# Kernel tuning notes

Hardware: AMD Instinct MI355X
Metric: run time of the kernel (lower is better)

## Reference

```python
import jax, jax.numpy as jnp
import numpy as np

B, S, E = 4, 1024, 1024
H = 16
HD = E // H  # 64
NEXP = 8
FF = 4 * E
EPS = 1e-5


def _ln(x, g, b):
    m = jnp.mean(x, axis=-1, keepdims=True)
    v = jnp.var(x, axis=-1, keepdims=True)
    return (x - m) * jax.lax.rsqrt(v + EPS) * g + b


def setup_inputs() -> dict:
    key = jax.random.key(0)
    ks = jax.random.split(key, 16)
    sd = 0.02
    inp = {
        "x": jax.random.normal(ks[0], (B, S, E), jnp.float32),
        # per-head Q/K/V linears, stacked over heads: [H, E, HD]
        "wq": jax.random.normal(ks[1], (H, E, HD), jnp.float32) * sd,
        "bq": jnp.zeros((H, HD), jnp.float32),
        "wk": jax.random.normal(ks[2], (H, E, HD), jnp.float32) * sd,
        "bk": jnp.zeros((H, HD), jnp.float32),
        "wv": jax.random.normal(ks[3], (H, E, HD), jnp.float32) * sd,
        "bv": jnp.zeros((H, HD), jnp.float32),
        "wp": jax.random.normal(ks[4], (E, E), jnp.float32) * sd,
        "bp": jnp.zeros((E,), jnp.float32),
        "ln1_g": jnp.ones((E,), jnp.float32),
        "ln1_b": jnp.zeros((E,), jnp.float32),
        "ln2_g": jnp.ones((E,), jnp.float32),
        "ln2_b": jnp.zeros((E,), jnp.float32),
        "wr": jax.random.normal(ks[5], (E, NEXP), jnp.float32) * sd,
        "br": jnp.zeros((NEXP,), jnp.float32),
        # experts stacked: [NEXP, E, FF], [NEXP, FF, E]
        "w1": jax.random.normal(ks[6], (NEXP, E, FF), jnp.float32) * sd,
        "b1": jnp.zeros((NEXP, FF), jnp.float32),
        "w2": jax.random.normal(ks[7], (NEXP, FF, E), jnp.float32) * sd,
        "b2": jnp.zeros((NEXP, E), jnp.float32),
    }
    return inp


def _block(x, wq, bq, wk, bk, wv, bv, wp, bp, ln1_g, ln1_b, ln2_g, ln2_b,
           wr, br, w1, b1, w2, b2):
    # --- multi-head causal attention (per-head Q/K/V, concat, project) ---
    q = jnp.einsum('bse,hed->bhsd', x, wq) + bq[None, :, None, :]
    k = jnp.einsum('bse,hed->bhsd', x, wk) + bk[None, :, None, :]
    v = jnp.einsum('bse,hed->bhsd', x, wv) + bv[None, :, None, :]
    scores = jnp.einsum('bhsd,bhtd->bhst', q, k) / jnp.sqrt(jnp.float32(HD))
    causal = jnp.tril(jnp.ones((S, S), bool))
    scores = jnp.where(causal[None, None], scores, -jnp.inf)
    attn = jax.nn.softmax(scores, axis=-1)
    heads = jnp.einsum('bhst,bhtd->bhsd', attn, v)
    # concat heads (dim order matches torch.cat over head list)
    cat = heads.transpose(0, 2, 1, 3).reshape(B, S, E)
    attn_out = cat @ wp + bp
    # --- residual + LN1 ---
    h = _ln(attn_out + x, ln1_g, ln1_b)
    # --- MoE: router probs weight ALL experts densely (indices unused) ---
    probs = jax.nn.softmax(h @ wr + br, axis=-1)  # [B,S,NEXP]
    mid = jax.nn.relu(jnp.einsum('bse,nef->bnsf', h, w1) + b1[None, :, None, :])
    eo = jnp.einsum('bnsf,nfe->bnse', mid, w2) + b2[None, :, None, :]
    moe_out = jnp.einsum('bnse,bsn->bse', eo, probs)
    # --- residual uses ORIGINAL inputs (as in source) + LN2 ---
    return _ln(moe_out + x, ln2_g, ln2_b)


def reference(x, wq, bq, wk, bk, wv, bv, wp, bp, ln1_g, ln1_b, ln2_g, ln2_b,
              wr, br, w1, b1, w2, b2):
    return _block(x, wq, bq, wk, bk, wv, bv, wp, bp, ln1_g, ln1_b,
                  ln2_g, ln2_b, wr, br, w1, b1, w2, b2)
```

## Files before the change

### kernel.cpp

```cpp
#include <hip/hip_runtime.h>
#include <hip/hip_bf16.h>

typedef unsigned short u16;
typedef unsigned int u32;
typedef __attribute__((ext_vector_type(8))) short bf16x8;
typedef __attribute__((ext_vector_type(4))) float f32x4;

#define DEV static __device__ __forceinline__

DEV u16 f2b(float f) {
  union { float f; u32 u; } v; v.f = f;
  return (u16)((v.u + 0x7fffu + ((v.u >> 16) & 1u)) >> 16);
}

DEV void gload16(const void* g, void* l) {
  __builtin_amdgcn_global_load_lds(
      (const __attribute__((address_space(1))) u32*)g,
      (__attribute__((address_space(3))) u32*)l, 16, 0, 0);
}

__global__ __launch_bounds__(256) void cvt_bf16(const float* __restrict__ s,
                                                u16* __restrict__ d) {
  const long i = ((long)blockIdx.x * 256 + threadIdx.x) * 4;
  const float4 v = *(const float4*)&s[i];
  ushort4 o;
  o.x = f2b(v.x); o.y = f2b(v.y); o.z = f2b(v.z); o.w = f2b(v.w);
  *(ushort4*)&d[i] = o;
}

__global__ __launch_bounds__(256) void tpose_bf16(const float* __restrict__ src,
                                                  u16* __restrict__ dst, int R,
                                                  int C, long sStride,
                                                  long dStride, long ldd) {
  __shared__ float tl[32][33];
  const float* s = src + (long)blockIdx.z * sStride;
  u16* d = dst + (long)blockIdx.z * dStride;
  const int c0 = blockIdx.x * 32, r0 = blockIdx.y * 32;
  const int tx = threadIdx.x, ty = threadIdx.y;
#pragma unroll
  for (int k = 0; k < 4; k++)
    tl[ty + k * 8][tx] = s[(long)(r0 + ty + k * 8) * C + c0 + tx];
  __syncthreads();
#pragma unroll
  for (int k = 0; k < 4; k++)
    d[(long)(c0 + ty + k * 8) * ldd + r0 + tx] = f2b(tl[tx][ty + k * 8]);
}

enum { EQKV, EPROJ, EFF1, EFF2, EFF2I };

template <int EPI>
__global__ __launch_bounds__(256, 2) void gemm_bt(
    const u16* __restrict__ A, const u16* __restrict__ Bt, int K, long lda,
    long ldb, const float* __restrict__ c0, const float* __restrict__ c1,
    const float* __restrict__ c2, const float* __restrict__ aux,
    float* __restrict__ fout, u16* __restrict__ o0, u16* __restrict__ o1,
    u16* __restrict__ o2, int ebase, long ldc) {
  __shared__ u16 As[8192], Bs[8192];
  long zc = 0;
  if constexpr (EPI == EFF2 || EPI == EFF2I) {
    const long z = blockIdx.z;
    A += z * (long)K;
    Bt += z * (long)K;
    fout += z * 4194304;
  }
  if constexpr (EPI == EFF1) {
    Bt += (long)blockIdx.z * 4194304;
    zc = (long)blockIdx.z * 4096;
  }
  const int tid = threadIdx.x;
  const int m0 = blockIdx.y * 128, n0 = blockIdx.x * 128;
  const int w = tid >> 6, l = tid & 63;
  const int wm = (w >> 1) * 64, wn = (w & 1) * 64;
  const int lr = l & 15, lh = l >> 4;
  f32x4 acc[4][4] = {};
  const u16* Ag = A + (long)(m0 + (tid >> 3)) * lda + (tid & 7) * 8;
  const u16* Bg = Bt + (long)(n0 + (tid >> 3)) * ldb + (tid & 7) * 8;
  for (int kt = 0; kt < K; kt += 64) {
    __syncthreads();
    gload16(Ag, As + tid * 8);
    gload16(Ag + 32 * lda, As + tid * 8 + 2048);
    gload16(Ag + 64 * lda, As + tid * 8 + 4096);
    gload16(Ag + 96 * lda, As + tid * 8 + 6144);
    gload16(Bg, Bs + tid * 8);
    gload16(Bg + 32 * ldb, Bs + tid * 8 + 2048);
    gload16(Bg + 64 * ldb, Bs + tid * 8 + 4096);
    gload16(Bg + 96 * ldb, Bs + tid * 8 + 6144);
    Ag += 64; Bg += 64;
    __syncthreads();
#pragma unroll
    for (int kk = 0; kk < 2; kk++) {
      bf16x8 af[4], bfr[4];
#pragma unroll
      for (int i = 0; i < 4; i++)
        af[i] = *(const bf16x8*)&As[(wm + i * 16 + lr) * 64 + kk * 32 + lh * 8];
#pragma unroll
      for (int j = 0; j < 4; j++)
        bfr[j] = *(const bf16x8*)&Bs[(wn + j * 16 + lr) * 64 + kk * 32 + lh * 8];
#pragma unroll
      for (int i = 0; i < 4; i++)
#pragma unroll
        for (int j = 0; j < 4; j++)
          acc[i][j] = __builtin_amdgcn_mfma_f32_16x16x32_bf16(
              af[i], bfr[j], acc[i][j], 0, 0, 0);
    }
  }
#pragma unroll
  for (int j = 0; j < 4; j++) {
    const int col = n0 + wn + j * 16 + lr;
#pragma unroll
    for (int i = 0; i < 4; i++)
#pragma unroll
      for (int r = 0; r < 4; r++) {
        const int row = m0 + wm + i * 16 + lh * 4 + r;
        float v = acc[i][j][r];
        if constexpr (EPI == EQKV) {
          const int which = col >> 10, hd = col & 1023;
          const float vb =
              v + ((which == 0) ? c0 : (which == 1) ? c1 : c2)[hd];
          const int b = row >> 10, s = row & 1023;
          const int h = hd >> 6, d = hd & 63;
          const long bh = b * 16 + h;
          if (which == 0)
            o0[(bh * 1024 + s) * 64 + d] = f2b(vb * 0.125f);
          else if (which == 1)
            o1[(bh * 1024 + s) * 64 + d] = f2b(vb);
          else
            o2[bh * 65536 + (long)d * 1024 + s] = f2b(vb);
        } else if constexpr (EPI == EPROJ) {
          const long idx = (long)row * 1024 + col;
          fout[idx] = v + c0[col] + aux[idx];
        } else if constexpr (EPI == EFF1) {
          const int e = ebase + blockIdx.z;
          const float t = v + c0[(long)e * 4096 + col];
          const float rl = t > 0.f ? t : 0.f;
          const float pw = aux[(long)row * 8 + e];
          o0[(long)row * ldc + zc + col] = f2b(rl * pw);
        } else {
          const long idx = (long)row * 1024 + col;
          if constexpr (EPI == EFF2I)
            fout[idx] = v;
          else
            fout[idx] = fout[idx] + v;
        }
      }
  }
}

__global__ __launch_bounds__(256) void attn_fwd(const u16* __restrict__ Qb,
                                                const u16* __restrict__ Kb,
                                                const u16* __restrict__ Vt,
                                                u16* __restrict__ Cat) {
  const int tid = threadIdx.x;
  const int w = tid >> 6, l = tid & 63;
  const int lr = l & 15, lh = l >> 4;
  const int bh = blockIdx.y;
  const int q0 = blockIdx.x * 64 + w * 16;
  const u16* Qp = Qb + (long)bh * 65536;
  const u16* Kp = Kb + (long)bh * 65536;
  const u16* Vp = Vt + (long)bh * 65536;
  const bf16x8 qf0 = *(const bf16x8*)&Qp[(q0 + lr) * 64 + lh * 8];
  const bf16x8 qf1 = *(const bf16x8*)&Qp[(q0 + lr) * 64 + 32 + lh * 8];
  const int q = q0 + lr;
  f32x4 o[4] = {};
  float m = -1e30f, ssum = 0.f;
  const int hi = lh >> 1;
  const int s0 = ((lh & 1) * 2) * 16 + lr;
  const int s1 = ((lh & 1) * 2 + 1) * 16 + lr;
  const int nkt = q0 / 32 + 1;
  for (int kt = 0; kt < nkt; kt++) {
    const int t0 = kt * 32;
    f32x4 sc[2];
#pragma unroll
    for (int ts = 0; ts < 2; ts++) {
      const bf16x8 kf0 = *(const bf16x8*)&Kp[(t0 + ts * 16 + lr) * 64 + lh * 8];
      const bf16x8 kf1 =
          *(const bf16x8*)&Kp[(t0 + ts * 16 + lr) * 64 + 32 + lh * 8];
      f32x4 c = {};
      c = __builtin_amdgcn_mfma_f32_16x16x32_bf16(kf0, qf0, c, 0, 0, 0);
      c = __builtin_amdgcn_mfma_f32_16x16x32_bf16(kf1, qf1, c, 0, 0, 0);
      sc[ts] = c;
    }
#pragma unroll
    for (int ts = 0; ts < 2; ts++)
#pragma unroll
      for (int r = 0; r < 4; r++)
        if (t0 + ts * 16 + lh * 4 + r > q) sc[ts][r] = -1e30f;
    float mt = fmaxf(fmaxf(fmaxf(sc[0][0], sc[0][1]), fmaxf(sc[0][2], sc[0][3])),
                     fmaxf(fmaxf(sc[1][0], sc[1][1]), fmaxf(sc[1][2], sc[1][3])));
    mt = fmaxf(mt, __shfl_xor(mt, 16));
    mt = fmaxf(mt, __shfl_xor(mt, 32));
    const float mnew = fmaxf(m, mt);
    const float scl = __expf(m - mnew);
    m = mnew;
    float p0[4], p1[4], ps = 0.f;
#pragma unroll
    for (int r = 0; r < 4; r++) {
      p0[r] = __expf(sc[0][r] - mnew);
      p1[r] = __expf(sc[1][r] - mnew);
      ps += p0[r] + p1[r];
    }
    ssum = ssum * scl + ps;
    u16 pb[8];
#pragma unroll
    for (int r = 0; r < 4; r++) {
      const float a0 = __shfl(p0[r], s0), b0 = __shfl(p1[r], s0);
      const float a1 = __shfl(p0[r], s1), b1 = __shfl(p1[r], s1);
      pb[r] = f2b(hi ? b0 : a0);
      pb[r + 4] = f2b(hi ? b1 : a1);
    }
#pragma unroll
    for (int dt = 0; dt < 4; dt++)
#pragma unroll
      for (int r = 0; r < 4; r++) o[dt][r] *= scl;
    const bf16x8 pf = *(const bf16x8*)pb;
    __builtin_amdgcn_s_setprio(1);
#pragma unroll
    for (int dt = 0; dt < 4; dt++) {
      const bf16x8 vf =
          *(const bf16x8*)&Vp[(dt * 16 + lr) * 1024 + t0 + lh * 8];
      o[dt] = __builtin_amdgcn_mfma_f32_16x16x32_bf16(vf, pf, o[dt], 0, 0, 0);
    }
    __builtin_amdgcn_s_setprio(0);
  }
  ssum += __shfl_xor(ssum, 16);
  ssum += __shfl_xor(ssum, 32);
  const float inv = 1.f / ssum;
  const int b = bh >> 4, h = bh & 15;
#pragma unroll
  for (int dt = 0; dt < 4; dt++) {
    ushort4 st;
    st.x = f2b(o[dt][0] * inv);
    st.y = f2b(o[dt][1] * inv);
    st.z = f2b(o[dt][2] * inv);
    st.w = f2b(o[dt][3] * inv);
    *(ushort4*)&Cat[((long)(b * 1024 + q)) * 1024 + h * 64 + dt * 16 + lh * 4] =
        st;
  }
}

DEV float wred(float v) {
#pragma unroll
  for (int d = 1; d < 64; d <<= 1) v += __shfl_xor(v, d);
  return v;
}

__global__ __launch_bounds__(256) void ln1_router(
    const float* __restrict__ in, const float* __restrict__ g,
    const float* __restrict__ bb, const float* __restrict__ wr,
    const float* __restrict__ br, u16* __restrict__ h,
    float* __restrict__ probs) {
  __shared__ float rs[4], rs2[4], rp[4][8];
  const int row = blockIdx.x, t = threadIdx.x;
  const int w = t >> 6, l = t & 63;
  const float4 v = *(const float4*)&in[(long)row * 1024 + t * 4];
  float s = v.x + v.y + v.z + v.w;
  float s2 = v.x * v.x + v.y * v.y + v.z * v.z + v.w * v.w;
  s = wred(s);
  s2 = wred(s2);
  if (l == 0) { rs[w] = s; rs2[w] = s2; }
  __syncthreads();
  const float S = rs[0] + rs[1] + rs[2] + rs[3];
  const float S2 = rs2[0] + rs2[1] + rs2[2] + rs2[3];
  const float mean = S * (1.f / 1024.f);
  const float var = S2 * (1.f / 1024.f) - mean * mean;
  const float rr = rsqrtf(var + 1e-5f);
  const float4 gv = *(const float4*)&g[t * 4];
  const float4 bv = *(const float4*)&bb[t * 4];
  float hv[4];
  hv[0] = (v.x - mean) * rr * gv.x + bv.x;
  hv[1] = (v.y - mean) * rr * gv.y + bv.y;
  hv[2] = (v.z - mean) * rr * gv.z + bv.z;
  hv[3] = (v.w - mean) * rr * gv.w + bv.w;
  ushort4 hb;
  hb.x = f2b(hv[0]); hb.y = f2b(hv[1]); hb.z = f2b(hv[2]); hb.w = f2b(hv[3]);
  *(ushort4*)&h[(long)row * 1024 + t * 4] = hb;
  float pr[8] = {};
  const float* wrp = wr + t * 4 * 8;
#pragma unroll
  for (int e = 0; e < 4; e++)
#pragma unroll
    for (int j = 0; j < 8; j++) pr[j] += hv[e] * wrp[e * 8 + j];
#pragma unroll
  for (int j = 0; j < 8; j++) pr[j] = wred(pr[j]);
  if (l == 0)
#pragma unroll
    for (int j = 0; j < 8; j++) rp[w][j] = pr[j];
  __syncthreads();
  if (t == 0) {
    float lg[8], mx = -1e30f;
#pragma unroll
    for (int j = 0; j < 8; j++) {
      lg[j] = rp[0][j] + rp[1][j] + rp[2][j] + rp[3][j] + br[j];
      mx = fmaxf(mx, lg[j]);
    }
    float sm = 0.f;
#pragma unroll
    for (int j = 0; j < 8; j++) {
      lg[j] = __expf(lg[j] - mx);
      sm += lg[j];
    }
    const float inv = 1.f / sm;
#pragma unroll
    for (int j = 0; j < 8; j++) probs[row * 8 + j] = lg[j] * inv;
  }
}

__global__ __launch_bounds__(256) void ln2_kernel(
    const float* __restrict__ moe, const float* __restrict__ xres,
    const float* __restrict__ probs, const float* __restrict__ b2,
    const float* __restrict__ g, const float* __restrict__ bb,
    float* __restrict__ out, int np) {
  __shared__ float rs[4], rs2[4];
  const int row = blockIdx.x, t = threadIdx.x;
  const int w = t >> 6, l = t & 63;
  const long base = (long)row * 1024 + t * 4;
  float4 v = *(const float4*)&xres[base];
  for (int z = 0; z < np; z++) {
    const float4 a = *(const float4*)&moe[(long)z * 4194304 + base];
    v.x += a.x; v.y += a.y; v.z += a.z; v.w += a.w;
  }
#pragma unroll
  for (int n = 0; n < 8; n++) {
    const float pw = probs[(long)row * 8 + n];
    const float4 bv4 = *(const float4*)&b2[n * 1024 + t * 4];
    v.x += pw * bv4.x; v.y += pw * bv4.y;
    v.z += pw * bv4.z; v.w += pw * bv4.w;
  }
  float s = v.x + v.y + v.z + v.w;
  float s2 = v.x * v.x + v.y * v.y + v.z * v.z + v.w * v.w;
  s = wred(s);
  s2 = wred(s2);
  if (l == 0) { rs[w] = s; rs2[w] = s2; }
  __syncthreads();
  const float S = rs[0] + rs[1] + rs[2] + rs[3];
  const float S2 = rs2[0] + rs2[1] + rs2[2] + rs2[3];
  const float mean = S * (1.f / 1024.f);
  const float var = S2 * (1.f / 1024.f) - mean * mean;
  const float rr = rsqrtf(var + 1e-5f);
  const float4 gv = *(const float4*)&g[t * 4];
  const float4 bv = *(const float4*)&bb[t * 4];
  float4 oo;
  oo.x = (v.x - mean) * rr * gv.x + bv.x;
  oo.y = (v.y - mean) * rr * gv.y + bv.y;
  oo.z = (v.z - mean) * rr * gv.z + bv.z;
  oo.w = (v.w - mean) * rr * gv.w + bv.w;
  *(float4*)&out[base] = oo;
}

extern "C" void kernel_launch(void* const* d_in, const int* in_sizes, int n_in,
                              void* d_out, int out_size, void* d_ws,
                              size_t ws_size, hipStream_t stream) {
  const float* x = (const float*)d_in[0];
  const float* wq = (const float*)d_in[1];
  const float* bq = (const float*)d_in[2];
  const float* wk = (const float*)d_in[3];
  const float* bk = (const float*)d_in[4];
  const float* wv = (const float*)d_in[5];
  const float* bv = (const float*)d_in[6];
  const float* wp = (const float*)d_in[7];
  const float* bp = (const float*)d_in[8];
  const float* g1 = (const float*)d_in[9];
  const float* be1 = (const float*)d_in[10];
  const float* g2 = (const float*)d_in[11];
  const float* be2 = (const float*)d_in[12];
  const float* wr = (const float*)d_in[13];
  const float* br = (const float*)d_in[14];
  const float* w1 = (const float*)d_in[15];
  const float* b1 = (const float*)d_in[16];
  const float* w2 = (const float*)d_in[17];
  const float* b2 = (const float*)d_in[18];
  float* out = (float*)d_out;

  char* p = (char*)d_ws;
  auto alloc = [&](size_t bytes) {
    char* r = p;
    p += (bytes + 255) & ~(size_t)255;
    return r;
  };
  u16* w1t = (u16*)alloc(67108864);
  u16* w2t2 = (u16*)alloc(67108864);
  u16* hb = (u16*)alloc(8388608);
  float* probs = (float*)alloc(131072);
  float* moe = (float*)alloc(33554432);
  float* resid1 = (float*)alloc(16777216);
  u16* xb = (u16*)alloc(8388608);
  u16* wqkvt = (u16*)alloc(6291456);
  u16* wpt = (u16*)alloc(2097152);
  u16* qb = (u16*)alloc(8388608);
  u16* kb = (u16*)alloc(8388608);
  u16* vt = (u16*)alloc(8388608);
  u16* cat = (u16*)alloc(8388608);
  const size_t need_fast = (size_t)((char*)qb - (char*)d_ws) + (size_t)268435456;
  const bool fast = ws_size >= need_fast;

  const dim3 tb(32, 8);
  cvt_bf16<<<4096, 256, 0, stream>>>(x, xb);
  tpose_bf16<<<dim3(2, 32, 16), tb, 0, stream>>>(wq, wqkvt, 1024, 64, 65536, 65536, 1024);
  tpose_bf16<<<dim3(2, 32, 16), tb, 0, stream>>>(wk, wqkvt + 1048576, 1024, 64, 65536, 65536, 1024);
  tpose_bf16<<<dim3(2, 32, 16), tb, 0, stream>>>(wv, wqkvt + 2097152, 1024, 64, 65536, 65536, 1024);
  tpose_bf16<<<dim3(32, 32, 1), tb, 0, stream>>>(wp, wpt, 1024, 1024, 0, 0, 1024);
  tpose_bf16<<<dim3(128, 32, 8), tb, 0, stream>>>(w1, w1t, 1024, 4096, 4194304, 4194304, 1024);
  tpose_bf16<<<dim3(32, 128, 8), tb, 0, stream>>>(w2, w2t2, 4096, 1024, 4194304, 4096, 32768);

  gemm_bt<EQKV><<<dim3(24, 32), 256, 0, stream>>>(
      xb, wqkvt, 1024, 1024, 1024, bq, bk, bv, nullptr, nullptr, qb, kb, vt,
      0, 0);
  attn_fwd<<<dim3(16, 64), 256, 0, stream>>>(qb, kb, vt, cat);
  gemm_bt<EPROJ><<<dim3(8, 32), 256, 0, stream>>>(
      cat, wpt, 1024, 1024, 1024, bp, nullptr, nullptr, x, resid1, nullptr,
      nullptr, nullptr, 0, 0);
  ln1_router<<<4096, 256, 0, stream>>>(resid1, g1, be1, wr, br, hb, probs);

  if (fast) {
    u16* mid = qb;
    gemm_bt<EFF1><<<dim3(32, 32, 8), 256, 0, stream>>>(
        hb, w1t, 1024, 1024, 1024, b1, nullptr, nullptr, probs, nullptr, mid,
        nullptr, nullptr, 0, 32768);
    gemm_bt<EFF2I><<<dim3(8, 32, 4), 256, 0, stream>>>(
        mid, w2t2, 8192, 32768, 32768, nullptr, nullptr, nullptr, nullptr,
        moe, nullptr, nullptr, nullptr, 0, 0);
    ln2_kernel<<<4096, 256, 0, stream>>>(moe, x, probs, b2, g2, be2, out, 4);
  } else {
    u16* mid = qb;
    for (int n = 0; n < 8; n++) {
      gemm_bt<EFF1><<<dim3(32, 32, 1), 256, 0, stream>>>(
          hb, w1t + (long)n * 4194304, 1024, 1024, 1024, b1, nullptr, nullptr,
          probs, nullptr, mid, nullptr, nullptr, n, 4096);
      if (n == 0)
        gemm_bt<EFF2I><<<dim3(8, 32, 2), 256, 0, stream>>>(
            mid, w2t2 + (long)n * 4096, 2048, 4096, 32768, nullptr, nullptr,
            nullptr, nullptr, moe, nullptr, nullptr, nullptr, 0, 0);
      else
        gemm_bt<EFF2><<<dim3(8, 32, 2), 256, 0, stream>>>(
            mid, w2t2 + (long)n * 4096, 2048, 4096, 32768, nullptr, nullptr,
            nullptr, nullptr, moe, nullptr, nullptr, nullptr, 0, 0);
    }
    ln2_kernel<<<4096, 256, 0, stream>>>(moe, x, probs, b2, g2, be2, out, 2);
  }
}
```

Baseline: 1.525 ms.

## Triple-buffer GEMM LDS with async prefetch and vectorize transpose stores

The GEMM main loop now keeps three 32-wide K slices in LDS and prefetches two tiles ahead with global_load_lds. It uses vmcnt waits and a single barrier per iteration instead of two, so global loads can overlap the MFMA work. It also raises launch bounds to 3 blocks per CU, sets wave priority around the MFMA block, and changes the transpose kernel to write 4 bf16 per thread as a vector. The cost is more LDS per block, a tighter register budget, and a fragile hand-written wait/barrier schedule that can race if the vmcnt counts are wrong.

```diff
diff --git a/kernel.cpp b/kernel.cpp
--- a/kernel.cpp
+++ b/kernel.cpp
@@ -37,25 +37,30 @@
   u16* d = dst + (long)blockIdx.z * dStride;
   const int c0 = blockIdx.x * 32, r0 = blockIdx.y * 32;
   const int tx = threadIdx.x, ty = threadIdx.y;
+  const int tid = ty * 32 + tx;
 #pragma unroll
   for (int k = 0; k < 4; k++)
     tl[ty + k * 8][tx] = s[(long)(r0 + ty + k * 8) * C + c0 + tx];
   __syncthreads();
-#pragma unroll
-  for (int k = 0; k < 4; k++)
-    d[(long)(c0 + ty + k * 8) * ldd + r0 + tx] = f2b(tl[tx][ty + k * 8]);
+  const int oc = tid >> 3, orb = (tid & 7) * 4;
+  ushort4 o;
+  o.x = f2b(tl[orb + 0][oc]);
+  o.y = f2b(tl[orb + 1][oc]);
+  o.z = f2b(tl[orb + 2][oc]);
+  o.w = f2b(tl[orb + 3][oc]);
+  *(ushort4*)&d[(long)(c0 + oc) * ldd + r0 + orb] = o;
 }
 
 enum { EQKV, EPROJ, EFF1, EFF2, EFF2I };
 
 template <int EPI>
-__global__ __launch_bounds__(256, 2) void gemm_bt(
+__global__ __launch_bounds__(256, 3) void gemm_bt(
     const u16* __restrict__ A, const u16* __restrict__ Bt, int K, long lda,
     long ldb, const float* __restrict__ c0, const float* __restrict__ c1,
     const float* __restrict__ c2, const float* __restrict__ aux,
     float* __restrict__ fout, u16* __restrict__ o0, u16* __restrict__ o1,
     u16* __restrict__ o2, int ebase, long ldc) {
-  __shared__ u16 As[8192], Bs[8192];
+  __shared__ u16 As[12288], Bs[12288];
   long zc = 0;
   if constexpr (EPI == EFF2 || EPI == EFF2I) {
     const long z = blockIdx.z;
@@ -73,37 +78,49 @@
   const int wm = (w >> 1) * 64, wn = (w & 1) * 64;
   const int lr = l & 15, lh = l >> 4;
   f32x4 acc[4][4] = {};
-  const u16* Ag = A + (long)(m0 + (tid >> 3)) * lda + (tid & 7) * 8;
-  const u16* Bg = Bt + (long)(n0 + (tid >> 3)) * ldb + (tid & 7) * 8;
-  for (int kt = 0; kt < K; kt += 64) {
-    __syncthreads();
-    gload16(Ag, As + tid * 8);
-    gload16(Ag + 32 * lda, As + tid * 8 + 2048);
-    gload16(Ag + 64 * lda, As + tid * 8 + 4096);
-    gload16(Ag + 96 * lda, As + tid * 8 + 6144);
-    gload16(Bg, Bs + tid * 8);
-    gload16(Bg + 32 * ldb, Bs + tid * 8 + 2048);
-    gload16(Bg + 64 * ldb, Bs + tid * 8 + 4096);
-    gload16(Bg + 96 * ldb, Bs + tid * 8 + 6144);
-    Ag += 64; Bg += 64;
-    __syncthreads();
-#pragma unroll
-    for (int kk = 0; kk < 2; kk++) {
-      bf16x8 af[4], bfr[4];
-#pragma unroll
-      for (int i = 0; i < 4; i++)
-        af[i] = *(const bf16x8*)&As[(wm + i * 16 + lr) * 64 + kk * 32 + lh * 8];
+  const u16* AgB = A + (long)(m0 + (tid >> 2)) * lda + (tid & 3) * 8;
+  const u16* BgB = Bt + (long)(n0 + (tid >> 2)) * ldb + (tid & 3) * 8;
+  const long rsA = 64 * lda, rsB = 64 * ldb;
+  u16* asd = As + tid * 8;
+  u16* bsd = Bs + tid * 8;
+  const int nt = K >> 5;
+  gload16(AgB, asd);             gload16(AgB + rsA, asd + 2048);
+  gload16(BgB, bsd);             gload16(BgB + rsB, bsd + 2048);
+  gload16(AgB + 32, asd + 4096); gload16(AgB + rsA + 32, asd + 6144);
+  gload16(BgB + 32, bsd + 4096); gload16(BgB + rsB + 32, bsd + 6144);
+  asm volatile("s_waitcnt vmcnt(4)" ::: "memory");
+  __builtin_amdgcn_sched_barrier(0);
+  __builtin_amdgcn_s_barrier();
+  __builtin_amdgcn_sched_barrier(0);
+  int oc = 0, on = 4096, ot = 8192;
+  for (int t = 0; t < nt; ++t) {
+    const int ks = (t + 2 < nt ? t + 2 : nt - 1) * 32;
+    gload16(AgB + ks, asd + ot);
+    gload16(AgB + rsA + ks, asd + ot + 2048);
+    gload16(BgB + ks, bsd + ot);
+    gload16(BgB + rsB + ks, bsd + ot + 2048);
+    bf16x8 af[4], bfr[4];
+#pragma unroll
+    for (int i = 0; i < 4; i++)
+      af[i] = *(const bf16x8*)&As[oc + (wm + i * 16 + lr) * 32 + lh * 8];
+#pragma unroll
+    for (int j = 0; j < 4; j++)
+      bfr[j] = *(const bf16x8*)&Bs[oc + (wn + j * 16 + lr) * 32 + lh * 8];
+    __builtin_amdgcn_s_setprio(1);
+#pragma unroll
+    for (int i = 0; i < 4; i++)
 #pragma unroll
       for (int j = 0; j < 4; j++)
-        bfr[j] = *(const bf16x8*)&Bs[(wn + j * 16 + lr) * 64 + kk * 32 + lh * 8];
-#pragma unroll
-      for (int i = 0; i < 4; i++)
-#pragma unroll
-        for (int j = 0; j < 4; j++)
-          acc[i][j] = __builtin_amdgcn_mfma_f32_16x16x32_bf16(
-              af[i], bfr[j], acc[i][j], 0, 0, 0);
-    }
-  }
+        acc[i][j] = __builtin_amdgcn_mfma_f32_16x16x32_bf16(af[i], bfr[j],
+                                                            acc[i][j], 0, 0, 0);
+    __builtin_amdgcn_s_setprio(0);
+    asm volatile("s_waitcnt vmcnt(4)" ::: "memory");
+    __builtin_amdgcn_sched_barrier(0);
+    __builtin_amdgcn_s_barrier();
+    __builtin_amdgcn_sched_barrier(0);
+    const int tmp = oc; oc = on; on = ot; ot = tmp;
+  }
+  asm volatile("s_waitcnt vmcnt(0)" ::: "memory");
 #pragma unroll
   for (int j = 0; j < 4; j++) {
     const int col = n0 + wn + j * 16 + lr;
```

After: 1.502 ms. About the same (-1.5%).
